# Kernel optimization log

Measured on AMD Instinct MI355X. Metric: run time of the kernel, lower is better.

## Reference

```python
import jax, jax.numpy as jnp
import numpy as np

BOUND = 2.7
N_REGIONS = 6
N_POINTS = N_REGIONS + 1
N_CHANNELS = 256


def setup_inputs() -> dict:
    key = jax.random.key(0)
    k1, k2 = jax.random.split(key)
    x = jax.random.normal(k1, (32, N_CHANNELS, 56, 56), dtype=jnp.float32)
    # points initialized like the module: relu(linspace(-bound, bound)) per channel,
    # plus a small perturbation so channels differ (learned-parameter stand-in)
    base = jax.nn.relu(jnp.linspace(-BOUND, BOUND, N_POINTS, dtype=jnp.float32))
    points = base[None, :] + 0.05 * jax.random.normal(k2, (N_CHANNELS, N_POINTS), dtype=jnp.float32)
    return {"x": x, "points": points}


def reference(x, points):
    # channelwise PWLU with fixed scalar bounds (learnable_bound=False)
    n_points = points.shape[-1]
    n_regions = n_points - 1
    n_channels = points.shape[0]
    region_length = (2.0 * BOUND) / n_regions  # scalar, as in the torch Real path

    x_normal = (x + BOUND) / region_length                      # [B,C,H,W]
    regions = jnp.clip(x_normal, 0.0, n_regions - 1).astype(jnp.int32)
    dists = x_normal - regions.astype(x.dtype)

    # pack per-channel indices into the flattened [C * n_regions] tables
    offsets = (jnp.arange(n_channels, dtype=jnp.int32) * n_regions).reshape(1, -1, 1, 1)
    idx = regions + offsets                                     # [B,C,H,W]

    left_points_tbl = points[:, :-1].reshape(-1)                # [C*R]
    diffs_tbl = (points[:, 1:] - points[:, :-1]).reshape(-1)    # [C*R]

    left_points = jnp.take(left_points_tbl, idx)
    diffs = jnp.take(diffs_tbl, idx)
    return left_points + dists * diffs
```

## Files before the change

### kernel.cpp

```cpp
#include <hip/hip_runtime.h>


#define N_PTS 7
#define VECS_PER_PLANE 784

__global__ __launch_bounds__(256) void pwlu_kernel(
    const float* __restrict__ x,
    const float* __restrict__ points,
    float* __restrict__ out,
    int nvec) {
  int i = blockIdx.x * blockDim.x + threadIdx.x;
  if (i >= nvec) return;

  const float4 xv = reinterpret_cast<const float4*>(x)[i];

  int c = (i / VECS_PER_PLANE) & 255;
  const float* __restrict__ p = points + c * N_PTS;

  float v[4] = {xv.x, xv.y, xv.z, xv.w};
  float r_[4];
#pragma unroll
  for (int k = 0; k < 4; ++k) {
    float xn = (v[k] + 2.7f) * (1.0f / 0.9f);
    float rc = fminf(fmaxf(xn, 0.0f), 5.0f);
    int r = (int)rc;
    float dist = xn - (float)r;
    float lp = p[r];
    float rp = p[r + 1];
    r_[k] = fmaf(dist, rp - lp, lp);
  }

  float4 ov;
  ov.x = r_[0]; ov.y = r_[1]; ov.z = r_[2]; ov.w = r_[3];
  reinterpret_cast<float4*>(out)[i] = ov;
}

extern "C" void kernel_launch(void* const* d_in, const int* in_sizes, int n_in,
                              void* d_out, int out_size, void* d_ws, size_t ws_size,
                              hipStream_t stream) {
  const float* x      = (const float*)d_in[0];
  const float* points = (const float*)d_in[1];
  float* out          = (float*)d_out;

  int n = in_sizes[0];
  int nvec = n / 4;
  int threads = 256;
  int blocks = (nvec + threads - 1) / threads;
  pwlu_kernel<<<blocks, threads, 0, stream>>>(x, points, out, nvec);
}
```

Measured before the change: 174.7 us.

## Replace table gather with branchless clamped-ramp sum, 8 elems/thread, nontemporal IO

Per-element dynamic indexing into the points table is replaced by a sum of clamped linear ramps using per-channel slope differences loaded once per thread. Each thread now processes two float4 vectors and uses nontemporal loads and stores to avoid cache pollution. This removes data-dependent gathers at the cost of more ALU per element and fewer threads in flight.

Result: slower. 178.3 us (+2.1%).

```diff
diff --git a/kernel.cpp b/kernel.cpp
--- a/kernel.cpp
+++ b/kernel.cpp
@@ -1,38 +1,52 @@
 #include <hip/hip_runtime.h>
 
 
+typedef float f4 __attribute__((ext_vector_type(4)));
+
+#define CHUNKS_PER_PLANE 392
 #define N_PTS 7
-#define VECS_PER_PLANE 784
 
 __global__ __launch_bounds__(256) void pwlu_kernel(
     const float* __restrict__ x,
     const float* __restrict__ points,
     float* __restrict__ out,
-    int nvec) {
+    int nchunk) {
   int i = blockIdx.x * blockDim.x + threadIdx.x;
-  if (i >= nvec) return;
+  if (i >= nchunk) return;
 
-  const float4 xv = reinterpret_cast<const float4*>(x)[i];
+  int c = (i / CHUNKS_PER_PLANE) & 255;
+  const float* __restrict__ p = points + c * N_PTS;
+  float p0 = p[0];
+  float d0 = p[1] - p0;
+  float d1 = p[2] - p[1];
+  float d2 = p[3] - p[2];
+  float d3 = p[4] - p[3];
+  float d4 = p[5] - p[4];
+  float d5 = p[6] - p[5];
 
-  int c = (i / VECS_PER_PLANE) & 255;
-  const float* __restrict__ p = points + c * N_PTS;
+  const f4* __restrict__ xv = reinterpret_cast<const f4*>(x) + (size_t)i * 2;
+  f4 a = __builtin_nontemporal_load(xv);
+  f4 b = __builtin_nontemporal_load(xv + 1);
 
-  float v[4] = {xv.x, xv.y, xv.z, xv.w};
-  float r_[4];
+  float v[8] = {a.x, a.y, a.z, a.w, b.x, b.y, b.z, b.w};
+  float r_[8];
 #pragma unroll
-  for (int k = 0; k < 4; ++k) {
-    float xn = (v[k] + 2.7f) * (1.0f / 0.9f);
-    float rc = fminf(fmaxf(xn, 0.0f), 5.0f);
-    int r = (int)rc;
-    float dist = xn - (float)r;
-    float lp = p[r];
-    float rp = p[r + 1];
-    r_[k] = fmaf(dist, rp - lp, lp);
+  for (int k = 0; k < 8; ++k) {
+    float xn = fmaf(v[k], 1.0f / 0.9f, 3.0f);
+    float acc = fmaf(d0, fminf(xn, 1.0f), p0);
+    acc = fmaf(d1, fminf(fmaxf(xn - 1.0f, 0.0f), 1.0f), acc);
+    acc = fmaf(d2, fminf(fmaxf(xn - 2.0f, 0.0f), 1.0f), acc);
+    acc = fmaf(d3, fminf(fmaxf(xn - 3.0f, 0.0f), 1.0f), acc);
+    acc = fmaf(d4, fminf(fmaxf(xn - 4.0f, 0.0f), 1.0f), acc);
+    acc = fmaf(d5, fmaxf(xn - 5.0f, 0.0f), acc);
+    r_[k] = acc;
   }
 
-  float4 ov;
-  ov.x = r_[0]; ov.y = r_[1]; ov.z = r_[2]; ov.w = r_[3];
-  reinterpret_cast<float4*>(out)[i] = ov;
+  f4 oa = {r_[0], r_[1], r_[2], r_[3]};
+  f4 ob = {r_[4], r_[5], r_[6], r_[7]};
+  f4* __restrict__ ov = reinterpret_cast<f4*>(out) + (size_t)i * 2;
+  __builtin_nontemporal_store(oa, ov);
+  __builtin_nontemporal_store(ob, ov + 1);
 }
 
 extern "C" void kernel_launch(void* const* d_in, const int* in_sizes, int n_in,
@@ -43,8 +57,8 @@
   float* out          = (float*)d_out;
 
   int n = in_sizes[0];
-  int nvec = n / 4;
+  int nchunk = n / 8;
   int threads = 256;
-  int blocks = (nvec + threads - 1) / threads;
-  pwlu_kernel<<<blocks, threads, 0, stream>>>(x, points, out, nvec);
+  int blocks = (nchunk + threads - 1) / threads;
+  pwlu_kernel<<<blocks, threads, 0, stream>>>(x, points, out, nchunk);
 }
```
